# Kernel tuning notes

Measured on AMD Instinct MI355X. Metric: run time of the kernel, lower is better.

## Reference

```python
import jax, jax.numpy as jnp
import numpy as np

B, N, H, D, T = 2, 512, 128, 128, 8  # batch, nodes, feat width, mid/out size, triplet fts
Z = 2 * H  # concat(node_fts, hidden)


def _lin_params(key, fan_in, fan_out):
    kw, kb = jax.random.split(key)
    scale = 1.0 / np.sqrt(fan_in)
    w = jax.random.uniform(kw, (fan_in, fan_out), jnp.float32, -scale, scale)
    b = jax.random.uniform(kb, (fan_out,), jnp.float32, -scale, scale)
    return w, b


def setup_inputs() -> dict:
    key = jax.random.key(0)
    ks = jax.random.split(key, 16)
    inp = {
        'node_fts': jax.random.normal(ks[0], (B, N, H), jnp.float32),
        'edge_fts': jax.random.normal(ks[1], (B, N, N, H), jnp.float32),
        'graph_fts': jax.random.normal(ks[2], (B, H), jnp.float32),
        'adj_mat': (jax.random.uniform(ks[3], (B, N, N)) < 0.5).astype(jnp.float32),
        'hidden': jax.random.normal(ks[4], (B, N, H), jnp.float32),
    }
    # message linears
    inp['Wm1'], inp['bm1'] = _lin_params(ks[5], Z, D)
    inp['Wm2'], inp['bm2'] = _lin_params(ks[6], Z, D)
    inp['Wme'], inp['bme'] = _lin_params(ks[7], H, D)
    inp['Wmg'], inp['bmg'] = _lin_params(ks[8], H, D)
    # output linears
    inp['Wo1'], inp['bo1'] = _lin_params(ks[9], Z, D)
    inp['Wo2'], inp['bo2'] = _lin_params(ks[10], D, D)
    # triplet linears
    inp['Wt1'], inp['bt1'] = _lin_params(ks[11], Z, T)
    inp['Wt2'], inp['bt2'] = _lin_params(ks[12], Z, T)
    inp['Wte'], inp['bte'] = _lin_params(ks[13], H, T)
    inp['Wtg'], inp['btg'] = _lin_params(ks[14], H, T)
    return inp


def reference(node_fts, edge_fts, graph_fts, adj_mat, hidden,
              Wm1, bm1, Wm2, bm2, Wme, bme, Wmg, bmg,
              Wo1, bo1, Wo2, bo2,
              Wt1, bt1, Wt2, bt2, Wte, bte, Wtg, btg):
    z = jnp.concatenate([node_fts, hidden], axis=-1)  # [b,n,2h]

    msg_1 = z @ Wm1 + bm1            # [b,n,d]
    msg_2 = z @ Wm2 + bm2            # [b,n,d]
    msg_e = edge_fts @ Wme + bme     # [b,n,n,d]
    msg_g = graph_fts @ Wmg + bmg    # [b,d]

    # triplet messages: broadcast pairwise sum -> relu, shape [b,n,n,t]
    tri = (z @ Wt1 + bt1)[:, None, :, :] \
        + (z @ Wt2 + bt2)[:, :, None, :] \
        + (edge_fts @ Wte + bte) \
        + (graph_fts @ Wtg + btg)[:, None, None, :]
    tri_msgs = jax.nn.relu(tri)

    # pairwise message broadcast-add, mask by adjacency, max over senders (axis 1)
    msgs = msg_1[:, None, :, :] + msg_2[:, :, None, :] + msg_e \
         + msg_g[:, None, None, :]                      # [b,n,n,d]
    msgs = jnp.max(msgs * adj_mat[..., None], axis=1)   # [b,n,d]

    ret = (z @ Wo1 + bo1) + (msgs @ Wo2 + bo2)           # [b,n,d]
    return (ret, tri_msgs)
```

## Files before the change

kernel.cpp:

```cpp
#include <hip/hip_runtime.h>
#include <hip/hip_bf16.h>

#define NB 2
#define NN 512
#define HH 128
#define DD 128
#define TT 8

#define WPACK_OFF 0
#define C_OFF     36864
#define BROW_OFF  561152
#define TC_OFF    1085440
#define TB_OFF    1118208
#define OC_OFF    1150976
#define PART_OFF  1675264
#define ZF_OFF    18452480

#define OUT_TRI   131072

typedef float f32x4 __attribute__((ext_vector_type(4)));
typedef short s16x8 __attribute__((ext_vector_type(8)));

__device__ __forceinline__ unsigned short f2bf(float f) {
    union { float f; unsigned int u; } x; x.f = f;
    unsigned int u = x.u;
    unsigned int r = (u + 0x7FFFu + ((u >> 16) & 1u)) >> 16;
    return (unsigned short)r;
}

__device__ __forceinline__ unsigned cvt2bf(float a, float b) {
#if __has_builtin(__builtin_amdgcn_cvt_pk_bf16_f32)
    auto r = __builtin_amdgcn_cvt_pk_bf16_f32(a, b);
    return __builtin_bit_cast(unsigned, r);
#else
    return (unsigned)f2bf(a) | ((unsigned)f2bf(b) << 16);
#endif
}

__global__ __launch_bounds__(256) void k0_precompute(
    const float* __restrict__ node, const float* __restrict__ hidden,
    const float* __restrict__ graph,
    const float* __restrict__ Wm1, const float* __restrict__ Wm2,
    const float* __restrict__ Wo1, const float* __restrict__ Wmg,
    const float* __restrict__ Wt1, const float* __restrict__ Wt2,
    const float* __restrict__ Wtg,
    const float* __restrict__ Wme, const float* __restrict__ Wte,
    const float* __restrict__ bm1, const float* __restrict__ bm2,
    const float* __restrict__ bme, const float* __restrict__ bmg,
    const float* __restrict__ bo1, const float* __restrict__ bo2,
    const float* __restrict__ bt1, const float* __restrict__ bt2,
    const float* __restrict__ bte, const float* __restrict__ btg,
    char* __restrict__ ws)
{
    const int bx = blockIdx.x, tid = threadIdx.x;
    if (bx == 512) {
        unsigned short* wp = (unsigned short*)(ws + WPACK_OFF);
        for (int idx = tid; idx < 16 * 144 * 8; idx += 256) {
            int j = idx & 7, tmp = idx >> 3;
            int n = tmp % 144, kq = tmp / 144;
            int k = kq * 8 + j;
            float v = 0.f;
            if (n < 128) v = Wme[k * 128 + n];
            else if (n < 136) v = Wte[k * 8 + (n - 128)];
            wp[idx] = f2bf(v);
        }
        return;
    }
    __shared__ float zs[2 * 260];
    const int row0 = bx * 2;
    const int b = row0 >> 9;
    #pragma unroll
    for (int e = 0; e < 2; e++) {
        int idx = e * 256 + tid;
        int rl = idx >> 8, col = idx & 255;
        float v = (col < 128) ? node[(row0 + rl) * 128 + col]
                              : hidden[(row0 + rl) * 128 + col - 128];
        zs[rl * 260 + col] = v;
    }
    __syncthreads();

    float* Cws = (float*)(ws + C_OFF);
    float* Bws = (float*)(ws + BROW_OFF);
    float* Ows = (float*)(ws + OC_OFF);
    float* TCw = (float*)(ws + TC_OFF);
    float* TBw = (float*)(ws + TB_OFF);

    const int d = tid & 127, half = tid >> 7;
    const int row = row0 + half;
    const float* z = zs + half * 260;
    float c = 0.f, q = 0.f, o = 0.f;
    #pragma unroll 8
    for (int k = 0; k < 256; k++) {
        float za = z[k];
        c = fmaf(za, Wm1[k * 128 + d], c);
        q = fmaf(za, Wm2[k * 128 + d], q);
        o = fmaf(za, Wo1[k * 128 + d], o);
    }
    float gm = 0.f;
    #pragma unroll 8
    for (int k = 0; k < 128; k++) gm = fmaf(graph[b * 128 + k], Wmg[k * 128 + d], gm);
    const float cb = gm + bm1[d] + bm2[d] + bme[d] + bmg[d];
    Cws[row * 128 + d] = c + cb;
    Bws[row * 128 + d] = q;
    Ows[row * 128 + d] = o + bo1[d] + bo2[d];

    if (tid < 32) {
        int rl = tid >> 4, t = (tid >> 1) & 7, which = tid & 1;
        const float* zr = zs + rl * 260;
        const float* W = which ? Wt2 : Wt1;
        float acc = 0.f;
        #pragma unroll 8
        for (int k = 0; k < 256; k++) acc = fmaf(zr[k], W[k * 8 + t], acc);
        int rg = row0 + rl;
        if (which == 0) {
            float gt = 0.f;
            #pragma unroll 8
            for (int k = 0; k < 128; k++) gt = fmaf(graph[b * 128 + k], Wtg[k * 8 + t], gt);
            TCw[rg * 8 + t] = acc + gt + bt1[t] + bt2[t] + bte[t] + btg[t];
        } else {
            TBw[rg * 8 + t] = acc;
        }
    }
}

__global__ __launch_bounds__(512, 2) void k2_main(
    const float* __restrict__ edge, const float* __restrict__ adj,
    char* __restrict__ ws, float* __restrict__ out)
{
    __shared__ float red[8][16][64];
    __shared__ int zflag[16];
    const int tid = threadIdx.x;
    const int jt = blockIdx.x, ic = blockIdx.y, b = blockIdx.z;
    const int j0 = jt * 16, i0 = ic * 64;

    const int lane = tid & 63, wave = tid >> 6;
    const int g = wave >> 2, sq = wave & 3;
    const int quad = lane >> 4, l15 = lane & 15;
    const int ntbase = g * 4;

    if (tid < 16) zflag[tid] = 0;
    __syncthreads();

    const float* Bws = (const float*)(ws + BROW_OFF);
    const float* TCw = (const float*)(ws + TC_OFF);
    const float* TBw = (const float*)(ws + TB_OFF);
    const s16x8* wp8 = (const s16x8*)(ws + WPACK_OFF);
    float* part = (float*)(ws + PART_OFF);
    int* Zws = (int*)(ws + ZF_OFF);

    s16x8 Bf[5][4];
    #pragma unroll
    for (int s = 0; s < 4; s++) {
        #pragma unroll
        for (int ntl = 0; ntl < 5; ntl++) {
            int nt = (ntl < 4) ? (ntbase + ntl) : 8;
            Bf[ntl][s] = wp8[(4 * s + quad) * 144 + nt * 16 + l15];
        }
    }

    const int jb = j0 + quad * 4;
    float TCf[4];
    #pragma unroll
    for (int r = 0; r < 4; r++)
        TCf[r] = (l15 < 8) ? TCw[(b * 512 + jb + r) * 8 + l15] : 0.f;

    float Mx[4][4];
    #pragma unroll
    for (int ntl = 0; ntl < 4; ntl++)
        #pragma unroll
        for (int r = 0; r < 4; r++) Mx[ntl][r] = -INFINITY;
    int anyz[4] = {0, 0, 0, 0};

    const int ig0 = i0 + sq * 16;
    const float* erow = edge + ((b * 512 + ig0) * 512 + j0 + l15) * 128 + quad * 8;

    float4 raw[2][8];
    float4 adjn[2];
    float brwn[2][4];
    float tbn[2];

    {
        #pragma unroll
        for (int s = 0; s < 4; s++) {
            raw[0][2 * s]     = *(const float4*)(erow + s * 32);
            raw[0][2 * s + 1] = *(const float4*)(erow + s * 32 + 4);
        }
        adjn[0] = *(const float4*)(adj + (b * 512 + ig0) * 512 + jb);
        const int br0 = (b * 512 + ig0) * 128;
        #pragma unroll
        for (int ntl = 0; ntl < 4; ntl++)
            brwn[0][ntl] = Bws[br0 + (ntbase + ntl) * 16 + l15];
        tbn[0] = (l15 < 8) ? TBw[(b * 512 + ig0) * 8 + l15] : 0.f;
    }

    #pragma unroll 2
    for (int ii = 0; ii < 16; ii++) {
        const int p = ii & 1, pn = p ^ 1;
        const int ig = ig0 + ii;

        s16x8 af[4];
        #pragma unroll
        for (int s = 0; s < 4; s++) {
            union { s16x8 v; unsigned u[4]; } pk;
            float4 pv = raw[p][2 * s], qv = raw[p][2 * s + 1];
            pk.u[0] = cvt2bf(pv.x, pv.y);
            pk.u[1] = cvt2bf(pv.z, pv.w);
            pk.u[2] = cvt2bf(qv.x, qv.y);
            pk.u[3] = cvt2bf(qv.z, qv.w);
            af[s] = pk.v;
        }

        if (ii < 15) {
            const float* ernx = erow + (ii + 1) * 65536;
            #pragma unroll
            for (int s = 0; s < 4; s++) {
                raw[pn][2 * s]     = *(const float4*)(ernx + s * 32);
                raw[pn][2 * s + 1] = *(const float4*)(ernx + s * 32 + 4);
            }
            const int ign = ig + 1;
            adjn[pn] = *(const float4*)(adj + (b * 512 + ign) * 512 + jb);
            const int brn = (b * 512 + ign) * 128;
            #pragma unroll
            for (int ntl = 0; ntl < 4; ntl++)
                brwn[pn][ntl] = Bws[brn + (ntbase + ntl) * 16 + l15];
            tbn[pn] = (l15 < 8) ? TBw[(b * 512 + ign) * 8 + l15] : 0.f;
        }

        f32x4 acc[5];
        #pragma unroll
        for (int ntl = 0; ntl < 5; ntl++) acc[ntl] = (f32x4){0.f, 0.f, 0.f, 0.f};
        #pragma unroll
        for (int s = 0; s < 4; s++) {
            #pragma unroll
            for (int ntl = 0; ntl < 5; ntl++)
                acc[ntl] = __builtin_amdgcn_mfma_f32_16x16x32_bf16(
                    af[s], Bf[ntl][s], acc[ntl], 0, 0, 0);
        }

        const float av[4] = {adjn[p].x, adjn[p].y, adjn[p].z, adjn[p].w};
        #pragma unroll
        for (int r = 0; r < 4; r++) {
            const int isz = (av[r] == 0.f);
            anyz[r] |= isz;
            #pragma unroll
            for (int ntl = 0; ntl < 4; ntl++) {
                float v = isz ? -INFINITY : (acc[ntl][r] + brwn[p][ntl]);
                Mx[ntl][r] = fmaxf(Mx[ntl][r], v);
            }
        }
        if (g == 1 && l15 < 8) {
            float* tout = out + OUT_TRI + ((b * 512 + ig) * 512 + jb) * 8 + l15;
            #pragma unroll
            for (int r = 0; r < 4; r++) {
                float tv = acc[4][r] + TCf[r] + tbn[p];
                tout[r * 8] = fmaxf(tv, 0.f);
            }
        }
    }

    if (g == 0 && l15 == 0) {
        #pragma unroll
        for (int r = 0; r < 4; r++)
            if (anyz[r]) atomicOr(&zflag[quad * 4 + r], 1);
    }
    #pragma unroll
    for (int ntl = 0; ntl < 4; ntl++)
        #pragma unroll
        for (int r = 0; r < 4; r++)
            red[wave][quad * 4 + r][ntl * 16 + l15] = Mx[ntl][r];
    __syncthreads();

    {
        const int q = tid;
        const int j = q >> 5, dq = q & 31;
        const int g2 = dq >> 4, c0 = (dq & 15) * 4;
        const float* r0p = &red[g2 * 4][j][c0];
        float4 m = *(const float4*)r0p;
        #pragma unroll
        for (int w = 1; w < 4; w++) {
            const float4 o = *(const float4*)&red[g2 * 4 + w][j][c0];
            m.x = fmaxf(m.x, o.x); m.y = fmaxf(m.y, o.y);
            m.z = fmaxf(m.z, o.z); m.w = fmaxf(m.w, o.w);
        }
        *(float4*)(part + ((b * 8 + ic) * 512 + j0 + j) * 128 + dq * 4) = m;
    }
    if (tid < 16) Zws[(b * 8 + ic) * 512 + j0 + tid] = zflag[tid];
}

__global__ __launch_bounds__(128) void k3_final(
    const char* __restrict__ ws, const float* __restrict__ Wo2,
    float* __restrict__ out)
{
    __shared__ float ms[128];
    const int bj = blockIdx.x, d = threadIdx.x;
    const int b = bj >> 9, j = bj & 511;
    const float* part = (const float*)(ws + PART_OFF);
    const int* Zws = (const int*)(ws + ZF_OFF);
    const float* Cws = (const float*)(ws + C_OFF);
    const float* Ows = (const float*)(ws + OC_OFF);

    const int rj = b * 512 + j;
    float m = -INFINITY;
    int zf = 0;
    #pragma unroll
    for (int ic = 0; ic < 8; ic++) {
        m = fmaxf(m, part[((b * 8 + ic) * 512 + j) * 128 + d]);
        zf |= Zws[(b * 8 + ic) * 512 + j];
    }
    float c = Cws[rj * 128 + d];
    float mm = fmaxf(m + c, zf ? 0.f : -INFINITY);
    ms[d] = mm;
    __syncthreads();
    float acc = Ows[rj * 128 + d];
    #pragma unroll 8
    for (int k = 0; k < 128; k++) acc = fmaf(ms[k], Wo2[k * 128 + d], acc);
    out[rj * 128 + d] = acc;
}

extern "C" void kernel_launch(void* const* d_in, const int* in_sizes, int n_in,
                              void* d_out, int out_size, void* d_ws, size_t ws_size,
                              hipStream_t stream) {
    const float* node   = (const float*)d_in[0];
    const float* edge   = (const float*)d_in[1];
    const float* graph  = (const float*)d_in[2];
    const float* adj    = (const float*)d_in[3];
    const float* hidden = (const float*)d_in[4];
    const float* Wm1 = (const float*)d_in[5];  const float* bm1 = (const float*)d_in[6];
    const float* Wm2 = (const float*)d_in[7];  const float* bm2 = (const float*)d_in[8];
    const float* Wme = (const float*)d_in[9];  const float* bme = (const float*)d_in[10];
    const float* Wmg = (const float*)d_in[11]; const float* bmg = (const float*)d_in[12];
    const float* Wo1 = (const float*)d_in[13]; const float* bo1 = (const float*)d_in[14];
    const float* Wo2 = (const float*)d_in[15]; const float* bo2 = (const float*)d_in[16];
    const float* Wt1 = (const float*)d_in[17]; const float* bt1 = (const float*)d_in[18];
    const float* Wt2 = (const float*)d_in[19]; const float* bt2 = (const float*)d_in[20];
    const float* Wte = (const float*)d_in[21]; const float* bte = (const float*)d_in[22];
    const float* Wtg = (const float*)d_in[23]; const float* btg = (const float*)d_in[24];
    float* out = (float*)d_out;
    char* ws = (char*)d_ws;

    k0_precompute<<<dim3(513), dim3(256), 0, stream>>>(
        node, hidden, graph, Wm1, Wm2, Wo1, Wmg, Wt1, Wt2, Wtg, Wme, Wte,
        bm1, bm2, bme, bmg, bo1, bo2, bt1, bt2, bte, btg, ws);
    k2_main<<<dim3(32, 8, 2), dim3(512), 0, stream>>>(edge, adj, ws, out);
    k3_final<<<dim3(1024), dim3(128), 0, stream>>>(ws, Wo2, out);
}
```

Baseline: 500.7 us.

## Stage edge tiles through LDS, split N across waves, rotate triplet MFMA

The main kernel now uses 256-thread blocks over 32 sender rows. Each block loads the edge tile cooperatively with coalesced float4 reads into double-buffered LDS, so one converted A fragment is shared by all four waves. Before, each wave group loaded its own edge rows into registers. Each wave now covers two output N-tiles, and the triplet MFMA rotates among the waves per row, which removes the LDS cross-wave max reduction. The cost is a __syncthreads per row and twice as many partial-max slices for the final kernel to combine.

```diff
diff --git a/kernel.cpp b/kernel.cpp
--- a/kernel.cpp
+++ b/kernel.cpp
@@ -14,9 +14,11 @@
 #define TB_OFF    1118208
 #define OC_OFF    1150976
 #define PART_OFF  1675264
-#define ZF_OFF    18452480
+#define ZF_OFF    10063872
 
 #define OUT_TRI   131072
+
+#define AP 132
 
 typedef float f32x4 __attribute__((ext_vector_type(4)));
 typedef short s16x8 __attribute__((ext_vector_type(8)));
@@ -123,23 +125,17 @@
     }
 }
 
-__global__ __launch_bounds__(512, 2) void k2_main(
+__global__ __launch_bounds__(256, 4) void k2_main(
     const float* __restrict__ edge, const float* __restrict__ adj,
     char* __restrict__ ws, float* __restrict__ out)
 {
-    __shared__ float red[8][16][64];
-    __shared__ int zflag[16];
+    __shared__ __align__(16) float As[2][16 * AP];
     const int tid = threadIdx.x;
     const int jt = blockIdx.x, ic = blockIdx.y, b = blockIdx.z;
-    const int j0 = jt * 16, i0 = ic * 64;
+    const int j0 = jt * 16, i0 = ic * 32;
 
     const int lane = tid & 63, wave = tid >> 6;
-    const int g = wave >> 2, sq = wave & 3;
     const int quad = lane >> 4, l15 = lane & 15;
-    const int ntbase = g * 4;
-
-    if (tid < 16) zflag[tid] = 0;
-    __syncthreads();
 
     const float* Bws = (const float*)(ws + BROW_OFF);
     const float* TCw = (const float*)(ws + TC_OFF);
@@ -148,14 +144,12 @@
     float* part = (float*)(ws + PART_OFF);
     int* Zws = (int*)(ws + ZF_OFF);
 
-    s16x8 Bf[5][4];
+    s16x8 Bf[2][4], Bt[4];
     #pragma unroll
     for (int s = 0; s < 4; s++) {
-        #pragma unroll
-        for (int ntl = 0; ntl < 5; ntl++) {
-            int nt = (ntl < 4) ? (ntbase + ntl) : 8;
-            Bf[ntl][s] = wp8[(4 * s + quad) * 144 + nt * 16 + l15];
-        }
+        Bf[0][s] = wp8[(4 * s + quad) * 144 + (2 * wave) * 16 + l15];
+        Bf[1][s] = wp8[(4 * s + quad) * 144 + (2 * wave + 1) * 16 + l15];
+        Bt[s]    = wp8[(4 * s + quad) * 144 + 128 + l15];
     }
 
     const int jb = j0 + quad * 4;
@@ -164,45 +158,52 @@
     for (int r = 0; r < 4; r++)
         TCf[r] = (l15 < 8) ? TCw[(b * 512 + jb + r) * 8 + l15] : 0.f;
 
-    float Mx[4][4];
-    #pragma unroll
-    for (int ntl = 0; ntl < 4; ntl++)
+    const int f0 = tid, f1 = tid + 256;
+    const int g0off = (f0 >> 5) * 128 + (f0 & 31) * 4;
+    const int g1off = (f1 >> 5) * 128 + (f1 & 31) * 4;
+    const int l0off = (f0 >> 5) * AP + (f0 & 31) * 4;
+    const int l1off = (f1 >> 5) * AP + (f1 & 31) * 4;
+
+    const size_t ebase = ((size_t)(b * 512 + i0) * 512 + j0) * 128;
+    {
+        const float* nb = edge + ebase;
+        *(float4*)&As[0][l0off] = *(const float4*)(nb + g0off);
+        *(float4*)&As[0][l1off] = *(const float4*)(nb + g1off);
+    }
+    __syncthreads();
+
+    float Mx[2][4];
+    #pragma unroll
+    for (int ntl = 0; ntl < 2; ntl++)
         #pragma unroll
         for (int r = 0; r < 4; r++) Mx[ntl][r] = -INFINITY;
     int anyz[4] = {0, 0, 0, 0};
 
-    const int ig0 = i0 + sq * 16;
-    const float* erow = edge + ((b * 512 + ig0) * 512 + j0 + l15) * 128 + quad * 8;
-
-    float4 raw[2][8];
-    float4 adjn[2];
-    float brwn[2][4];
-    float tbn[2];
-
-    {
+    const int c0 = (2 * wave) * 16 + l15, c1 = c0 + 16;
+
+    for (int ii = 0; ii < 32; ii++) {
+        const int p = ii & 1, pn = p ^ 1;
+        const int ig = i0 + ii;
+        const int rowb = b * 512 + ig;
+
+        float4 st0, st1;
+        if (ii < 31) {
+            const float* nb = edge + ebase + (size_t)(ii + 1) * 65536;
+            st0 = *(const float4*)(nb + g0off);
+            st1 = *(const float4*)(nb + g1off);
+        }
+        const float4 adjv = *(const float4*)(adj + (size_t)rowb * 512 + jb);
+        const float brw0 = Bws[rowb * 128 + c0];
+        const float brw1 = Bws[rowb * 128 + c1];
+        const float tb   = TBw[rowb * 8 + (l15 & 7)];
+
+        s16x8 af[4];
+        const float* ap = &As[p][l15 * AP + quad * 8];
         #pragma unroll
         for (int s = 0; s < 4; s++) {
-            raw[0][2 * s]     = *(const float4*)(erow + s * 32);
-            raw[0][2 * s + 1] = *(const float4*)(erow + s * 32 + 4);
-        }
-        adjn[0] = *(const float4*)(adj + (b * 512 + ig0) * 512 + jb);
-        const int br0 = (b * 512 + ig0) * 128;
-        #pragma unroll
-        for (int ntl = 0; ntl < 4; ntl++)
-            brwn[0][ntl] = Bws[br0 + (ntbase + ntl) * 16 + l15];
-        tbn[0] = (l15 < 8) ? TBw[(b * 512 + ig0) * 8 + l15] : 0.f;
-    }
-
-    #pragma unroll 2
-    for (int ii = 0; ii < 16; ii++) {
-        const int p = ii & 1, pn = p ^ 1;
-        const int ig = ig0 + ii;
-
-        s16x8 af[4];
-        #pragma unroll
-        for (int s = 0; s < 4; s++) {
+            float4 pv = *(const float4*)(ap + s * 32);
+            float4 qv = *(const float4*)(ap + s * 32 + 4);
             union { s16x8 v; unsigned u[4]; } pk;
-            float4 pv = raw[p][2 * s], qv = raw[p][2 * s + 1];
             pk.u[0] = cvt2bf(pv.x, pv.y);
             pk.u[1] = cvt2bf(pv.z, pv.w);
             pk.u[2] = cvt2bf(qv.x, qv.y);
@@ -210,81 +211,54 @@
             af[s] = pk.v;
         }
 
-        if (ii < 15) {
-            const float* ernx = erow + (ii + 1) * 65536;
+        f32x4 acc0 = (f32x4){0.f, 0.f, 0.f, 0.f};
+        f32x4 acc1 = (f32x4){0.f, 0.f, 0.f, 0.f};
+        #pragma unroll
+        for (int s = 0; s < 4; s++) {
+            acc0 = __builtin_amdgcn_mfma_f32_16x16x32_bf16(af[s], Bf[0][s], acc0, 0, 0, 0);
+            acc1 = __builtin_amdgcn_mfma_f32_16x16x32_bf16(af[s], Bf[1][s], acc1, 0, 0, 0);
+        }
+        const int trimine = ((ii & 3) == wave);
+        f32x4 acct = (f32x4){0.f, 0.f, 0.f, 0.f};
+        if (trimine) {
             #pragma unroll
-            for (int s = 0; s < 4; s++) {
-                raw[pn][2 * s]     = *(const float4*)(ernx + s * 32);
-                raw[pn][2 * s + 1] = *(const float4*)(ernx + s * 32 + 4);
-            }
-            const int ign = ig + 1;
-            adjn[pn] = *(const float4*)(adj + (b * 512 + ign) * 512 + jb);
-            const int brn = (b * 512 + ign) * 128;
-            #pragma unroll
-            for (int ntl = 0; ntl < 4; ntl++)
-                brwn[pn][ntl] = Bws[brn + (ntbase + ntl) * 16 + l15];
-            tbn[pn] = (l15 < 8) ? TBw[(b * 512 + ign) * 8 + l15] : 0.f;
-        }
-
-        f32x4 acc[5];
-        #pragma unroll
-        for (int ntl = 0; ntl < 5; ntl++) acc[ntl] = (f32x4){0.f, 0.f, 0.f, 0.f};
-        #pragma unroll
-        for (int s = 0; s < 4; s++) {
-            #pragma unroll
-            for (int ntl = 0; ntl < 5; ntl++)
-                acc[ntl] = __builtin_amdgcn_mfma_f32_16x16x32_bf16(
-                    af[s], Bf[ntl][s], acc[ntl], 0, 0, 0);
-        }
-
-        const float av[4] = {adjn[p].x, adjn[p].y, adjn[p].z, adjn[p].w};
+            for (int s = 0; s < 4; s++)
+                acct = __builtin_amdgcn_mfma_f32_16x16x32_bf16(af[s], Bt[s], acct, 0, 0, 0);
+        }
+
+        if (ii < 31) {
+            *(float4*)&As[pn][l0off] = st0;
+            *(float4*)&As[pn][l1off] = st1;
+        }
+
+        const float av[4] = {adjv.x, adjv.y, adjv.z, adjv.w};
         #pragma unroll
         for (int r = 0; r < 4; r++) {
             const int isz = (av[r] == 0.f);
             anyz[r] |= isz;
+            Mx[0][r] = fmaxf(Mx[0][r], isz ? -INFINITY : (acc0[r] + brw0));
+            Mx[1][r] = fmaxf(Mx[1][r], isz ? -INFINITY : (acc1[r] + brw1));
+        }
+        if (trimine && l15 < 8) {
+            float* tout = out + OUT_TRI + ((size_t)rowb * 512 + jb) * 8 + l15;
             #pragma unroll
-            for (int ntl = 0; ntl < 4; ntl++) {
-                float v = isz ? -INFINITY : (acc[ntl][r] + brwn[p][ntl]);
-                Mx[ntl][r] = fmaxf(Mx[ntl][r], v);
-            }
-        }
-        if (g == 1 && l15 < 8) {
-            float* tout = out + OUT_TRI + ((b * 512 + ig) * 512 + jb) * 8 + l15;
-            #pragma unroll
-            for (int r = 0; r < 4; r++) {
-                float tv = acc[4][r] + TCf[r] + tbn[p];
-                tout[r * 8] = fmaxf(tv, 0.f);
-            }
-        }
-    }
-
-    if (g == 0 && l15 == 0) {
+            for (int r = 0; r < 4; r++)
+                tout[r * 8] = fmaxf(acct[r] + TCf[r] + tb, 0.f);
+        }
+        __syncthreads();
+    }
+
+    #pragma unroll
+    for (int r = 0; r < 4; r++) {
+        const size_t pb = ((size_t)(b * 16 + ic) * 512 + jb + r) * 128;
+        part[pb + c0] = Mx[0][r];
+        part[pb + c1] = Mx[1][r];
+    }
+    if (wave == 0 && l15 == 0) {
         #pragma unroll
         for (int r = 0; r < 4; r++)
-            if (anyz[r]) atomicOr(&zflag[quad * 4 + r], 1);
-    }
-    #pragma unroll
-    for (int ntl = 0; ntl < 4; ntl++)
-        #pragma unroll
-        for (int r = 0; r < 4; r++)
-            red[wave][quad * 4 + r][ntl * 16 + l15] = Mx[ntl][r];
-    __syncthreads();
-
-    {
-        const int q = tid;
-        const int j = q >> 5, dq = q & 31;
-        const int g2 = dq >> 4, c0 = (dq & 15) * 4;
-        const float* r0p = &red[g2 * 4][j][c0];
-        float4 m = *(const float4*)r0p;
-        #pragma unroll
-        for (int w = 1; w < 4; w++) {
-            const float4 o = *(const float4*)&red[g2 * 4 + w][j][c0];
-            m.x = fmaxf(m.x, o.x); m.y = fmaxf(m.y, o.y);
-            m.z = fmaxf(m.z, o.z); m.w = fmaxf(m.w, o.w);
-        }
-        *(float4*)(part + ((b * 8 + ic) * 512 + j0 + j) * 128 + dq * 4) = m;
-    }
-    if (tid < 16) Zws[(b * 8 + ic) * 512 + j0 + tid] = zflag[tid];
+            Zws[(b * 16 + ic) * 512 + jb + r] = anyz[r];
+    }
 }
 
 __global__ __launch_bounds__(128) void k3_final(
@@ -303,9 +277,9 @@
     float m = -INFINITY;
     int zf = 0;
     #pragma unroll
-    for (int ic = 0; ic < 8; ic++) {
-        m = fmaxf(m, part[((b * 8 + ic) * 512 + j) * 128 + d]);
-        zf |= Zws[(b * 8 + ic) * 512 + j];
+    for (int ic = 0; ic < 16; ic++) {
+        m = fmaxf(m, part[((size_t)(b * 16 + ic) * 512 + j) * 128 + d]);
+        zf |= Zws[(b * 16 + ic) * 512 + j];
     }
     float c = Cws[rj * 128 + d];
     float mm = fmaxf(m + c, zf ? 0.f : -INFINITY);
@@ -341,6 +315,6 @@
     k0_precompute<<<dim3(513), dim3(256), 0, stream>>>(
         node, hidden, graph, Wm1, Wm2, Wo1, Wmg, Wt1, Wt2, Wtg, Wme, Wte,
         bm1, bm2, bme, bmg, bo1, bo2, bt1, bt2, bte, btg, ws);
-    k2_main<<<dim3(32, 8, 2), dim3(512), 0, stream>>>(edge, adj, ws, out);
+    k2_main<<<dim3(32, 16, 2), dim3(256), 0, stream>>>(edge, adj, ws, out);
     k3_final<<<dim3(1024), dim3(128), 0, stream>>>(ws, Wo2, out);
 }
```

New measurement: 472.5 us. -5.6%, faster.
